# Performance work log

Measured on AMD Instinct MI355X. Metric: run time of the kernel, lower is better.

The kernel has to match this reference:

```python
import jax, jax.numpy as jnp
import numpy as np

# Arbitrary non-contiguous kernel tap offsets (constructor arg sk_ind)
SK_IND = np.array([-512, -256, -128, -96, -64, -48, -32, -24, -16, -12, -8, -6,
                   -4, -3, -2, -1, 0, 1, 2, 3, 4, 6, 8, 12, 16, 24, 32, 48,
                   64, 96, 128, 256], dtype=np.int32)
IN_CHANNELS = 64
OUT_CHANNELS = 64
BATCH = 16
INPUT_LEN = 4096


def setup_inputs() -> dict:
    key = jax.random.key(0)
    k1, k2 = jax.random.split(key)
    x = jax.random.normal(k1, (BATCH, IN_CHANNELS, INPUT_LEN), dtype=jnp.float32)
    sk_weights = jax.random.normal(k2, (OUT_CHANNELS, IN_CHANNELS, SK_IND.shape[0]), dtype=jnp.float32)
    return {"x": x, "sk_weights": sk_weights}


def reference(x, sk_weights):
    # x: [B, Cin, L]; sk_weights: [Cout, Cin, K]
    B, C, L = x.shape
    low_pad = max(-int(SK_IND.min()), 0)   # zeros consumed by negative taps
    high_pad = max(int(SK_IND.max()), 0)   # zeros consumed by positive taps
    # Original pads zeros AFTER the signal: [x, zeros(high_pad), zeros(low_pad)];
    # negative numpy indices then wrap into the trailing low_pad zeros.
    padded = jnp.concatenate([x, jnp.zeros((B, C, high_pad + low_pad), x.dtype)], axis=-1)
    padded_len = L + high_pad + low_pad
    idx = SK_IND[:, None] + np.arange(L)                 # [K, L], static
    idx = np.where(idx < 0, padded_len + idx, idx)       # emulate numpy negative-index wrap
    gathered = padded[:, :, idx]                          # [B, Cin, K, L]
    # Per-position GEMM: contract over (Cin, K)
    return jnp.einsum('oik,bikl->bol', sk_weights, gathered)  # [B, Cout, L]
```

## Files before the change

### kernel.cpp

```cpp
#include <hip/hip_runtime.h>


#define B_    16
#define CIN   64
#define COUT  64
#define LEN   4096
#define PAD_LO 512
#define PAD_HI 256
#define LPAD  (LEN + PAD_LO + PAD_HI)
#define NTAP  32
#define WOFF  131072

typedef float f32x4 __attribute__((ext_vector_type(4)));
typedef short bf16x8_s __attribute__((ext_vector_type(8)));
typedef __bf16 bf16x8_b __attribute__((ext_vector_type(8)));
typedef unsigned short u16x8 __attribute__((ext_vector_type(8)));

template <typename V>
static __device__ inline auto mfma_16x16x32_bf16(V a, V b, f32x4 c, int)
    -> decltype(__builtin_amdgcn_mfma_f32_16x16x32_bf16(a, b, c, 0, 0, 0)) {
  return __builtin_amdgcn_mfma_f32_16x16x32_bf16(a, b, c, 0, 0, 0);
}
template <typename V>
static __device__ inline f32x4 mfma_16x16x32_bf16(V a, V b, f32x4 c, long) {
  return __builtin_amdgcn_mfma_f32_16x16x32_bf16(
      __builtin_bit_cast(bf16x8_b, a), __builtin_bit_cast(bf16x8_b, b), c, 0, 0, 0);
}

static __device__ inline unsigned short f32_to_bf16_rne(float f) {
  unsigned int u = __builtin_bit_cast(unsigned int, f);
  u += 0x7fffu + ((u >> 16) & 1u);
  return (unsigned short)(u >> 16);
}

static __device__ inline void async_copy16(const void* g, void* l) {
  __builtin_amdgcn_global_load_lds((const __attribute__((address_space(1))) unsigned int*)g,
                                   (__attribute__((address_space(3))) unsigned int*)l, 16, 0, 0);
}

__global__ __launch_bounds__(256) void prep_x(const float* __restrict__ x,
                                              unsigned short* __restrict__ xp) {
  __shared__ float tile[64][65];
  const int b = blockIdx.y;
  const int lp0 = blockIdx.x * 64;
  const int tid = threadIdx.x;
  const bool data = (lp0 >= PAD_LO) && (lp0 < PAD_LO + LEN);
  if (data) {
    const int l0 = lp0 - PAD_LO;
#pragma unroll
    for (int it = 0; it < 4; ++it) {
      const int pidx = it * 256 + tid;
      const int il = pidx >> 4;
      const int lq = (pidx & 15) * 4;
      const float4 v = *(const float4*)&x[(size_t)(b * CIN + il) * LEN + l0 + lq];
      tile[lq + 0][il] = v.x;
      tile[lq + 1][il] = v.y;
      tile[lq + 2][il] = v.z;
      tile[lq + 3][il] = v.w;
    }
  }
  __syncthreads();
#pragma unroll
  for (int it = 0; it < 2; ++it) {
    const int pidx = it * 256 + tid;
    const int ll = pidx >> 3;
    const int i8 = (pidx & 7) * 8;
    u16x8 v = {0, 0, 0, 0, 0, 0, 0, 0};
    if (data) {
#pragma unroll
      for (int j = 0; j < 8; ++j) v[j] = f32_to_bf16_rne(tile[ll][i8 + j]);
    }
    *(u16x8*)&xp[(size_t)(b * LPAD + lp0 + ll) * CIN + i8] = v;
  }
}

__global__ __launch_bounds__(256) void prep_w(const float* __restrict__ w,
                                              unsigned short* __restrict__ wf) {
  const int e = blockIdx.x * 256 + threadIdx.x;
  const int j = e & 7;
  const int lane = (e >> 3) & 63;
  const int m = (e >> 9) & 3;
  const int c = (e >> 11) & 1;
  const int t = e >> 12;
  const int q = lane >> 4, r = lane & 15;
  const int o = m * 16 + r;
  const int i = c * 32 + q * 8 + j;
  wf[e] = f32_to_bf16_rne(w[(size_t)(o * CIN + i) * NTAP + t]);
}

__global__ __launch_bounds__(512, 2) void sconv_main(const unsigned short* __restrict__ xp,
                                                     const unsigned short* __restrict__ wf,
                                                     float* __restrict__ out) {
  constexpr int TAP[NTAP] = {-512, -256, -128, -96, -64, -48, -32, -24, -16, -12, -8,
                             -6,   -4,   -3,   -2,  -1,  0,   1,   2,   3,   4,  6,
                             8,    12,   16,   24,  32,  48,  64,  96,  128, 256};
  __shared__ alignas(16) char smem[WOFF + 16384];

  const int id = blockIdx.x;
  const int b = (id & 7) * 2 + (id >> 7);
  const int l0 = ((id >> 3) & 15) * 256;
  const int lb = l0 + PAD_LO;
  const int tid = threadIdx.x;
  const int wv = tid >> 6, lane = tid & 63;
  const int q = lane >> 4, r = lane & 15;
  const int lh = wv >> 1, ch = wv & 1;

  const char* xbase = (const char*)xp + ((size_t)b * LPAD + lb) * (CIN * 2);
  const char* wbase = (const char*)wf;

  auto stageW = [&](int t) {
    async_copy16(wbase + t * 8192 + (wv * 64 + lane) * 16,
                 smem + WOFF + (t & 1) * 8192 + wv * 1024);
  };
  auto stageB = [&](int a0, int ng) {
    for (int g = wv; g < ng; g += 8) {
      const int ra = a0 + g * 8 + (lane >> 3);
      const int cs = (lane & 7) ^ (ra & 7);
      const int sb = (lb + a0 + g * 8) & 1023;
      async_copy16(xbase + (ptrdiff_t)ra * 128 + cs * 16, smem + sb * 128);
    }
  };

  f32x4 acc[4][4] = {};
  bf16x8_s Ab[2][4], Bb[2][4];

  auto readFrags = [&](int tt, int p) {
    const char* Wb = smem + WOFF + (tt & 1) * 8192 + ch * 4096;
#pragma unroll
    for (int m = 0; m < 4; ++m)
      Ab[p][m] = *(const bf16x8_s*)(Wb + m * 1024 + lane * 16);
    const int e = (TAP[tt] + r) & 7;
#pragma unroll
    for (int n = 0; n < 4; ++n) {
      const int slot = (lb + TAP[tt] + lh * 64 + 16 * n + r) & 1023;
      Bb[p][n] = *(const bf16x8_s*)(smem + slot * 128 + (((ch * 4 + q) ^ e) << 4));
    }
  };

  stageW(0);
  stageW(1);
  stageB(-512, 64);
  __syncthreads();
  readFrags(0, 0);

#pragma unroll
  for (int t = 0; t < NTAP; ++t) {
    __syncthreads();
    if (t + 2 < NTAP) {
      stageW(t + 2);
      const int dstart = TAP[t + 1] + 256;
      const int dend = TAP[t + 2] + 256;
      const int a0 = dstart & ~7;
      stageB(a0, (dend - a0 + 7) >> 3);
    }
    __builtin_amdgcn_sched_barrier(0);
    if (t + 1 < NTAP) readFrags(t + 1, (t + 1) & 1);
    __builtin_amdgcn_sched_barrier(0);
    const int p = t & 1;
#pragma unroll
    for (int m = 0; m < 4; ++m)
#pragma unroll
      for (int n = 0; n < 4; ++n)
        acc[m][n] = mfma_16x16x32_bf16(Ab[p][m], Bb[p][n], acc[m][n], 0);
  }

  __syncthreads();
  if (ch == 1) {
#pragma unroll
    for (int m = 0; m < 4; ++m)
#pragma unroll
      for (int n = 0; n < 4; ++n)
        *(f32x4*)(smem + lh * 16384 + ((m * 4 + n) * 64 + lane) * 16) = acc[m][n];
  }
  __syncthreads();
  if (ch == 0) {
#pragma unroll
    for (int m = 0; m < 4; ++m)
#pragma unroll
      for (int n = 0; n < 4; ++n) {
        const f32x4 other = *(const f32x4*)(smem + lh * 16384 + ((m * 4 + n) * 64 + lane) * 16);
        const f32x4 v = acc[m][n] + other;
#pragma unroll
        for (int d = 0; d < 4; ++d) {
          const int o = 16 * m + 4 * q + d;
          const int l = l0 + lh * 64 + 16 * n + r;
          out[((size_t)b * COUT + o) * LEN + l] = v[d];
        }
      }
  }
}

extern "C" void kernel_launch(void* const* d_in, const int* in_sizes, int n_in,
                              void* d_out, int out_size, void* d_ws, size_t ws_size,
                              hipStream_t stream) {
  const float* x = (const float*)d_in[0];
  const float* w = (const float*)d_in[1];
  float* out = (float*)d_out;

  unsigned short* xp = (unsigned short*)d_ws;
  unsigned short* wfp = xp + (size_t)B_ * LPAD * CIN;

  prep_x<<<dim3(LPAD / 64, B_), 256, 0, stream>>>(x, xp);
  prep_w<<<dim3((NTAP * 2 * 4 * 64 * 8) / 256), 256, 0, stream>>>(w, wfp);
  sconv_main<<<dim3(256), 512, 0, stream>>>(xp, wfp, out);
}
```

Baseline: 93.53 us.

## Fuse weight prep into x prep and load weights directly to registers with 4-tap sync groups

Folds the weight-conversion kernel into the x transpose kernel, using the idle pad-region blocks, which saves one launch. In the main kernel, weight fragments are now loaded straight from global memory into registers instead of being staged through LDS. The input-window staging moves from one barrier per tap to one per group of four taps, so there are fewer __syncthreads. The trade-off is global-load latency on the weight path, which relies on L2 hits and register double-buffering, plus larger staging chunks per group.

```diff
diff --git a/kernel.cpp b/kernel.cpp
--- a/kernel.cpp
+++ b/kernel.cpp
@@ -9,7 +9,6 @@
 #define PAD_HI 256
 #define LPAD  (LEN + PAD_LO + PAD_HI)
 #define NTAP  32
-#define WOFF  131072
 
 typedef float f32x4 __attribute__((ext_vector_type(4)));
 typedef short bf16x8_s __attribute__((ext_vector_type(8)));
@@ -38,8 +37,10 @@
                                    (__attribute__((address_space(3))) unsigned int*)l, 16, 0, 0);
 }
 
-__global__ __launch_bounds__(256) void prep_x(const float* __restrict__ x,
-                                              unsigned short* __restrict__ xp) {
+__global__ __launch_bounds__(256) void prep_xw(const float* __restrict__ x,
+                                               const float* __restrict__ w,
+                                               unsigned short* __restrict__ xp,
+                                               unsigned short* __restrict__ wf) {
   __shared__ float tile[64][65];
   const int b = blockIdx.y;
   const int lp0 = blockIdx.x * 64;
@@ -58,6 +59,20 @@
       tile[lq + 2][il] = v.z;
       tile[lq + 3][il] = v.w;
     }
+  } else if (lp0 < PAD_LO) {
+    const int base = (b * 8 + blockIdx.x) * 1024;
+#pragma unroll
+    for (int it = 0; it < 4; ++it) {
+      const int e = base + it * 256 + tid;
+      const int j = e & 7;
+      const int lane = (e >> 3) & 63;
+      const int m = (e >> 9) & 3;
+      const int c = (e >> 11) & 1;
+      const int t = e >> 12;
+      const int o = m * 16 + (lane & 15);
+      const int i = c * 32 + (lane >> 4) * 8 + j;
+      wf[e] = f32_to_bf16_rne(w[(size_t)(o * CIN + i) * NTAP + t]);
+    }
   }
   __syncthreads();
 #pragma unroll
@@ -74,27 +89,13 @@
   }
 }
 
-__global__ __launch_bounds__(256) void prep_w(const float* __restrict__ w,
-                                              unsigned short* __restrict__ wf) {
-  const int e = blockIdx.x * 256 + threadIdx.x;
-  const int j = e & 7;
-  const int lane = (e >> 3) & 63;
-  const int m = (e >> 9) & 3;
-  const int c = (e >> 11) & 1;
-  const int t = e >> 12;
-  const int q = lane >> 4, r = lane & 15;
-  const int o = m * 16 + r;
-  const int i = c * 32 + q * 8 + j;
-  wf[e] = f32_to_bf16_rne(w[(size_t)(o * CIN + i) * NTAP + t]);
-}
-
 __global__ __launch_bounds__(512, 2) void sconv_main(const unsigned short* __restrict__ xp,
                                                      const unsigned short* __restrict__ wf,
                                                      float* __restrict__ out) {
   constexpr int TAP[NTAP] = {-512, -256, -128, -96, -64, -48, -32, -24, -16, -12, -8,
                              -6,   -4,   -3,   -2,  -1,  0,   1,   2,   3,   4,  6,
                              8,    12,   16,   24,  32,  48,  64,  96,  128, 256};
-  __shared__ alignas(16) char smem[WOFF + 16384];
+  __shared__ alignas(16) char smem[131072];
 
   const int id = blockIdx.x;
   const int b = (id & 7) * 2 + (id >> 7);
@@ -108,10 +109,6 @@
   const char* xbase = (const char*)xp + ((size_t)b * LPAD + lb) * (CIN * 2);
   const char* wbase = (const char*)wf;
 
-  auto stageW = [&](int t) {
-    async_copy16(wbase + t * 8192 + (wv * 64 + lane) * 16,
-                 smem + WOFF + (t & 1) * 8192 + wv * 1024);
-  };
   auto stageB = [&](int a0, int ng) {
     for (int g = wv; g < ng; g += 8) {
       const int ra = a0 + g * 8 + (lane >> 3);
@@ -121,47 +118,52 @@
     }
   };
 
+  bf16x8_s Wreg[2][4], Breg[2][4];
   f32x4 acc[4][4] = {};
-  bf16x8_s Ab[2][4], Bb[2][4];
-
-  auto readFrags = [&](int tt, int p) {
-    const char* Wb = smem + WOFF + (tt & 1) * 8192 + ch * 4096;
+
+  auto loadW = [&](int tt, int p) {
+    const char* src = wbase + tt * 8192 + ch * 4096 + lane * 16;
 #pragma unroll
     for (int m = 0; m < 4; ++m)
-      Ab[p][m] = *(const bf16x8_s*)(Wb + m * 1024 + lane * 16);
+      Wreg[p][m] = *(const bf16x8_s*)(src + m * 1024);
+  };
+  auto readB = [&](int tt, int p) {
     const int e = (TAP[tt] + r) & 7;
 #pragma unroll
     for (int n = 0; n < 4; ++n) {
       const int slot = (lb + TAP[tt] + lh * 64 + 16 * n + r) & 1023;
-      Bb[p][n] = *(const bf16x8_s*)(smem + slot * 128 + (((ch * 4 + q) ^ e) << 4));
+      Breg[p][n] = *(const bf16x8_s*)(smem + slot * 128 + (((ch * 4 + q) ^ e) << 4));
     }
   };
 
-  stageW(0);
-  stageW(1);
-  stageB(-512, 64);
-  __syncthreads();
-  readFrags(0, 0);
-
-#pragma unroll
-  for (int t = 0; t < NTAP; ++t) {
+  loadW(0, 0);
+  stageB(-512, 84);
+
+#pragma unroll
+  for (int g = 0; g < 8; ++g) {
     __syncthreads();
-    if (t + 2 < NTAP) {
-      stageW(t + 2);
-      const int dstart = TAP[t + 1] + 256;
-      const int dend = TAP[t + 2] + 256;
+    readB(4 * g, 0);
+    if (g < 7) {
+      const int dstart = TAP[4 * g + 3] + 256;
+      const int dend = TAP[4 * g + 7] + 256;
       const int a0 = dstart & ~7;
       stageB(a0, (dend - a0 + 7) >> 3);
     }
     __builtin_amdgcn_sched_barrier(0);
-    if (t + 1 < NTAP) readFrags(t + 1, (t + 1) & 1);
-    __builtin_amdgcn_sched_barrier(0);
-    const int p = t & 1;
-#pragma unroll
-    for (int m = 0; m < 4; ++m)
-#pragma unroll
-      for (int n = 0; n < 4; ++n)
-        acc[m][n] = mfma_16x16x32_bf16(Ab[p][m], Bb[p][n], acc[m][n], 0);
+#pragma unroll
+    for (int u = 0; u < 4; ++u) {
+      const int t = 4 * g + u, p = t & 1;
+      if (t + 1 < NTAP) {
+        loadW(t + 1, p ^ 1);
+        if ((t + 1) & 3) readB(t + 1, p ^ 1);
+      }
+      __builtin_amdgcn_sched_barrier(0);
+#pragma unroll
+      for (int m = 0; m < 4; ++m)
+#pragma unroll
+        for (int n = 0; n < 4; ++n)
+          acc[m][n] = mfma_16x16x32_bf16(Wreg[p][m], Breg[p][n], acc[m][n], 0);
+    }
   }
 
   __syncthreads();
@@ -200,7 +202,6 @@
   unsigned short* xp = (unsigned short*)d_ws;
   unsigned short* wfp = xp + (size_t)B_ * LPAD * CIN;
 
-  prep_x<<<dim3(LPAD / 64, B_), 256, 0, stream>>>(x, xp);
-  prep_w<<<dim3((NTAP * 2 * 4 * 64 * 8) / 256), 256, 0, stream>>>(w, wfp);
+  prep_xw<<<dim3(LPAD / 64, B_), 256, 0, stream>>>(x, w, xp, wfp);
   sconv_main<<<dim3(256), 512, 0, stream>>>(xp, wfp, out);
 }
```

Measured after the change: 89.88 us. 1.04x faster.
